# Performance work log

Measured on AMD Instinct MI355X. Metric: run time of the kernel, lower is better.

The kernel has to match this reference:

```python
import jax, jax.numpy as jnp
import numpy as np

B, T, RNN_DIM, ENC_DIM, ATT_DIM, NFILT, KSIZE = 256, 1024, 1024, 512, 128, 32, 31
PAD = (KSIZE - 1) // 2


def setup_inputs() -> dict:
    key = jax.random.key(0)
    ks = jax.random.split(key, 10)
    attn = jax.random.uniform(ks[3], (B, T), dtype=jnp.float32)
    attn = attn / jnp.sum(attn, axis=1, keepdims=True)  # previous-step alignment (sums to 1)
    return {
        "query": jax.random.normal(ks[0], (B, RNN_DIM), dtype=jnp.float32),
        "memory": jax.random.normal(ks[1], (B, T, ENC_DIM), dtype=jnp.float32),
        "processed_memory": jax.random.normal(ks[2], (B, T, ATT_DIM), dtype=jnp.float32),
        "attn_weights": attn,
        "attn_weights_cum": jax.random.uniform(ks[4], (B, T), dtype=jnp.float32),
        "memory_lengths": jax.random.randint(ks[5], (B,), T // 2, T + 1),
        "conv_w": jax.random.normal(ks[6], (NFILT, 2, KSIZE), dtype=jnp.float32) * 0.1,
        "W_loc": jax.random.normal(ks[7], (ATT_DIM, NFILT), dtype=jnp.float32) * 0.1,
        "W_q": jax.random.normal(ks[8], (ATT_DIM, RNN_DIM), dtype=jnp.float32) * 0.03,
        "v_w": jax.random.normal(ks[9], (1, ATT_DIM), dtype=jnp.float32) * 0.1,
        "v_b": jnp.zeros((1,), dtype=jnp.float32),
    }


def reference(query, memory, processed_memory, attn_weights, attn_weights_cum,
              memory_lengths, conv_w, W_loc, W_q, v_w, v_b):
    Tlen = memory.shape[1]
    # [B, 2, T]: stack prev + cumulative alignments
    cat = jnp.stack([attn_weights, attn_weights_cum], axis=1)
    # location conv: Conv1d(2 -> NFILT, k=31, same padding, no bias) -> [B, NFILT, T]
    loc = jax.lax.conv_general_dilated(
        cat, conv_w, window_strides=(1,), padding=[(PAD, PAD)],
        dimension_numbers=("NCH", "OIH", "NCH"))
    # location_dense: [B, T, ATT_DIM]
    processed_location = jnp.einsum("bct,ac->bta", loc, W_loc)
    # query projection: [B, 1, ATT_DIM]
    processed_query = (query @ W_q.T)[:, None, :]
    # additive energies: v . tanh(q + loc + mem) -> [B, T]
    hidden = jnp.tanh(processed_query + processed_location + processed_memory)
    energies = jnp.einsum("bta,a->bt", hidden, v_w[0]) + v_b[0]
    # mask padded positions (pos >= length) with -inf
    mask = jnp.arange(Tlen)[None, :] >= memory_lengths[:, None]
    energies = jnp.where(mask, -jnp.inf, energies)
    new_attn = jax.nn.softmax(energies, axis=1)
    new_cum = attn_weights_cum + new_attn
    # context: [B, ENC_DIM]
    context = jnp.einsum("bt,bte->be", new_attn, memory)
    return context, new_attn, new_cum
```

## Files before the change

### kernel.cpp

```cpp
#include <hip/hip_runtime.h>
#include <math.h>

#define Bc 256
#define Tc 1024
#define RNN_DIMc 1024
#define ENC_DIMc 512
#define ATT_DIMc 128
#define NFILTc 32
#define KSIZEc 31
#define PADc 15

typedef float f4v __attribute__((ext_vector_type(4)));

__device__ __forceinline__ float fast_tanh(float x) {
    x = fminf(15.f, fmaxf(-15.f, x));
    float z = __expf(2.f * x);
    return (z - 1.f) / (z + 1.f);
}

__device__ __forceinline__ float wave_reduce_max(float x) {
#pragma unroll
    for (int off = 32; off > 0; off >>= 1) x = fmaxf(x, __shfl_xor(x, off, 64));
    return x;
}

__device__ __forceinline__ float wave_reduce_sum(float x) {
#pragma unroll
    for (int off = 32; off > 0; off >>= 1) x += __shfl_xor(x, off, 64);
    return x;
}

__global__ __launch_bounds__(128) void qproj_k(const float* __restrict__ query,
                                               const float* __restrict__ W_q,
                                               float* __restrict__ pq) {
    const int b = blockIdx.x;
    __shared__ float q[RNN_DIMc];
    for (int i = threadIdx.x; i < RNN_DIMc; i += 128) q[i] = query[b * RNN_DIMc + i];
    __syncthreads();
    const float* w = W_q + (size_t)threadIdx.x * RNN_DIMc;
    float acc = 0.f;
#pragma unroll 4
    for (int r = 0; r < RNN_DIMc; r += 4) {
        float4 wv = *(const float4*)(w + r);
        acc = fmaf(wv.x, q[r + 0], acc);
        acc = fmaf(wv.y, q[r + 1], acc);
        acc = fmaf(wv.z, q[r + 2], acc);
        acc = fmaf(wv.w, q[r + 3], acc);
    }
    pq[b * ATT_DIMc + threadIdx.x] = acc;
}

__global__ __launch_bounds__(1024) void lsa_fused(
    const float* __restrict__ memory, const float* __restrict__ pm,
    const float* __restrict__ attn_w, const float* __restrict__ cum_w,
    const int* __restrict__ lens, const float* __restrict__ conv_w,
    const float* __restrict__ W_loc, const float* __restrict__ pq_g,
    const float* __restrict__ v_w, const float* __restrict__ v_b,
    float* __restrict__ ctx, float* __restrict__ out_attn, float* __restrict__ out_cum) {
    const int b = blockIdx.x;
    const int tid = threadIdx.x;
    const int len = lens[b];

    __shared__ float s_pq[ATT_DIMc];
    __shared__ float s_win0[Tc + 2 * PADc];
    __shared__ float s_win1[Tc + 2 * PADc];
    __shared__ float s_attn[Tc];
    __shared__ float s_redm[16];
    __shared__ float s_reds[16];
    __shared__ float s_scratch[8][ENC_DIMc];

    if (tid < ATT_DIMc) s_pq[tid] = pq_g[b * ATT_DIMc + tid];
    for (int i = tid; i < Tc + 2 * PADc; i += 1024) {
        int tt = i - PADc;
        bool ok = (tt >= 0) && (tt < Tc);
        s_win0[i] = ok ? attn_w[b * Tc + tt] : 0.f;
        s_win1[i] = ok ? cum_w[b * Tc + tt] : 0.f;
    }
    __syncthreads();

    const int t = tid;
    float e = -INFINITY;
    if (t < len) {
        float loc[NFILTc];
#pragma unroll
        for (int f = 0; f < NFILTc; ++f) loc[f] = 0.f;
        for (int k = 0; k < KSIZEc; ++k) {
            const float wa = s_win0[t + k];
            const float wc = s_win1[t + k];
#pragma unroll
            for (int f = 0; f < NFILTc; ++f) {
                loc[f] = fmaf(conv_w[f * (2 * KSIZEc) + k], wa, loc[f]);
                loc[f] = fmaf(conv_w[f * (2 * KSIZEc) + KSIZEc + k], wc, loc[f]);
            }
        }

        const float* pmrow = pm + ((size_t)(b * Tc + t)) * ATT_DIMc;
        float acc = 0.f;
#pragma unroll 2
        for (int a = 0; a < ATT_DIMc; a += 4) {
            const f4v pmv = __builtin_nontemporal_load((const f4v*)(pmrow + a));
            const float* wl = W_loc + a * NFILTc;
            float pl0 = 0.f, pl1 = 0.f, pl2 = 0.f, pl3 = 0.f;
#pragma unroll
            for (int f = 0; f < NFILTc; ++f) {
                float lf = loc[f];
                pl0 = fmaf(wl[f], lf, pl0);
                pl1 = fmaf(wl[NFILTc + f], lf, pl1);
                pl2 = fmaf(wl[2 * NFILTc + f], lf, pl2);
                pl3 = fmaf(wl[3 * NFILTc + f], lf, pl3);
            }
            acc = fmaf(v_w[a + 0], fast_tanh(s_pq[a + 0] + pl0 + pmv.x), acc);
            acc = fmaf(v_w[a + 1], fast_tanh(s_pq[a + 1] + pl1 + pmv.y), acc);
            acc = fmaf(v_w[a + 2], fast_tanh(s_pq[a + 2] + pl2 + pmv.z), acc);
            acc = fmaf(v_w[a + 3], fast_tanh(s_pq[a + 3] + pl3 + pmv.w), acc);
        }
        e = acc + v_b[0];
    }

    {
        float m = wave_reduce_max(e);
        if ((tid & 63) == 0) s_redm[tid >> 6] = m;
        __syncthreads();
        float bm = s_redm[0];
#pragma unroll
        for (int j = 1; j < 16; ++j) bm = fmaxf(bm, s_redm[j]);

        float p = __expf(e - bm);
        float s = wave_reduce_sum(p);
        if ((tid & 63) == 0) s_reds[tid >> 6] = s;
        __syncthreads();
        float tot = 0.f;
#pragma unroll
        for (int j = 0; j < 16; ++j) tot += s_reds[j];
        float na = p * (1.f / tot);

        out_attn[b * Tc + t] = na;
        out_cum[b * Tc + t] = s_win1[t + PADc] + na;
        s_attn[t] = na;
    }
    __syncthreads();

    {
        const int tr = tid >> 7;
        const int e4 = (tid & 127) * 4;
        const float* mb = memory + (size_t)b * Tc * ENC_DIMc;
        f4v acc = {0.f, 0.f, 0.f, 0.f};
#pragma unroll 4
        for (int tt = tr; tt < len; tt += 8) {
            const float w = s_attn[tt];
            const f4v mv = __builtin_nontemporal_load((const f4v*)(mb + (size_t)tt * ENC_DIMc + e4));
            acc.x = fmaf(w, mv.x, acc.x);
            acc.y = fmaf(w, mv.y, acc.y);
            acc.z = fmaf(w, mv.z, acc.z);
            acc.w = fmaf(w, mv.w, acc.w);
        }
        *(f4v*)&s_scratch[tr][e4] = acc;
    }
    __syncthreads();
    if (tid < ENC_DIMc) {
        float s = 0.f;
#pragma unroll
        for (int j = 0; j < 8; ++j) s += s_scratch[j][tid];
        ctx[b * ENC_DIMc + tid] = s;
    }
}

extern "C" void kernel_launch(void* const* d_in, const int* in_sizes, int n_in,
                              void* d_out, int out_size, void* d_ws, size_t ws_size,
                              hipStream_t stream) {
    const float* query  = (const float*)d_in[0];
    const float* memory = (const float*)d_in[1];
    const float* pm     = (const float*)d_in[2];
    const float* attn_w = (const float*)d_in[3];
    const float* cum_w  = (const float*)d_in[4];
    const int*   lens   = (const int*)d_in[5];
    const float* conv_w = (const float*)d_in[6];
    const float* W_loc  = (const float*)d_in[7];
    const float* W_q    = (const float*)d_in[8];
    const float* v_w    = (const float*)d_in[9];
    const float* v_b    = (const float*)d_in[10];

    float* out      = (float*)d_out;
    float* ctx      = out;
    float* out_attn = out + Bc * ENC_DIMc;
    float* out_cum  = out + Bc * ENC_DIMc + Bc * Tc;

    float* pq = (float*)d_ws;

    qproj_k<<<Bc, 128, 0, stream>>>(query, W_q, pq);
    lsa_fused<<<Bc, 1024, 0, stream>>>(memory, pm, attn_w, cum_w, lens,
                                       conv_w, W_loc, pq, v_w, v_b,
                                       ctx, out_attn, out_cum);
}
```

Before: 816.1 us.

## Fuse query projection into main attention kernel and widen context reduction

Removes the separate qproj kernel and computes the query projection inside each block: 8 threads per attention dim split the 1024-wide dot product and combine partials with wave shuffles. This drops one kernel launch and the global round trip for the projected query. The context stage now uses 16 row groups with 8 contiguous floats per thread instead of 8 row groups with 4, which means more loads in flight but doubles the shared-memory scratch to 32KB and may lower occupancy.

```diff
diff --git a/kernel.cpp b/kernel.cpp
--- a/kernel.cpp
+++ b/kernel.cpp
@@ -30,51 +30,54 @@
     return x;
 }
 
-__global__ __launch_bounds__(128) void qproj_k(const float* __restrict__ query,
-                                               const float* __restrict__ W_q,
-                                               float* __restrict__ pq) {
-    const int b = blockIdx.x;
-    __shared__ float q[RNN_DIMc];
-    for (int i = threadIdx.x; i < RNN_DIMc; i += 128) q[i] = query[b * RNN_DIMc + i];
-    __syncthreads();
-    const float* w = W_q + (size_t)threadIdx.x * RNN_DIMc;
-    float acc = 0.f;
-#pragma unroll 4
-    for (int r = 0; r < RNN_DIMc; r += 4) {
-        float4 wv = *(const float4*)(w + r);
-        acc = fmaf(wv.x, q[r + 0], acc);
-        acc = fmaf(wv.y, q[r + 1], acc);
-        acc = fmaf(wv.z, q[r + 2], acc);
-        acc = fmaf(wv.w, q[r + 3], acc);
-    }
-    pq[b * ATT_DIMc + threadIdx.x] = acc;
-}
-
 __global__ __launch_bounds__(1024) void lsa_fused(
-    const float* __restrict__ memory, const float* __restrict__ pm,
-    const float* __restrict__ attn_w, const float* __restrict__ cum_w,
-    const int* __restrict__ lens, const float* __restrict__ conv_w,
-    const float* __restrict__ W_loc, const float* __restrict__ pq_g,
-    const float* __restrict__ v_w, const float* __restrict__ v_b,
-    float* __restrict__ ctx, float* __restrict__ out_attn, float* __restrict__ out_cum) {
+    const float* __restrict__ query, const float* __restrict__ memory,
+    const float* __restrict__ pm, const float* __restrict__ attn_w,
+    const float* __restrict__ cum_w, const int* __restrict__ lens,
+    const float* __restrict__ conv_w, const float* __restrict__ W_loc,
+    const float* __restrict__ W_q, const float* __restrict__ v_w,
+    const float* __restrict__ v_b, float* __restrict__ ctx,
+    float* __restrict__ out_attn, float* __restrict__ out_cum) {
     const int b = blockIdx.x;
     const int tid = threadIdx.x;
     const int len = lens[b];
 
+    __shared__ float s_q[RNN_DIMc];
     __shared__ float s_pq[ATT_DIMc];
     __shared__ float s_win0[Tc + 2 * PADc];
     __shared__ float s_win1[Tc + 2 * PADc];
     __shared__ float s_attn[Tc];
     __shared__ float s_redm[16];
     __shared__ float s_reds[16];
-    __shared__ float s_scratch[8][ENC_DIMc];
-
-    if (tid < ATT_DIMc) s_pq[tid] = pq_g[b * ATT_DIMc + tid];
+    __shared__ float s_ctx[16][ENC_DIMc];
+
+    s_q[tid] = query[b * RNN_DIMc + tid];
     for (int i = tid; i < Tc + 2 * PADc; i += 1024) {
         int tt = i - PADc;
         bool ok = (tt >= 0) && (tt < Tc);
         s_win0[i] = ok ? attn_w[b * Tc + tt] : 0.f;
         s_win1[i] = ok ? cum_w[b * Tc + tt] : 0.f;
+    }
+    __syncthreads();
+
+    {
+        const int a = tid >> 3;
+        const int c = tid & 7;
+        const float* w = W_q + (size_t)a * RNN_DIMc;
+        float acc = 0.f;
+#pragma unroll 4
+        for (int j = 0; j < 32; ++j) {
+            const int r = c * 4 + j * 32;
+            float4 wv = *(const float4*)(w + r);
+            acc = fmaf(wv.x, s_q[r + 0], acc);
+            acc = fmaf(wv.y, s_q[r + 1], acc);
+            acc = fmaf(wv.z, s_q[r + 2], acc);
+            acc = fmaf(wv.w, s_q[r + 3], acc);
+        }
+        acc += __shfl_xor(acc, 1, 64);
+        acc += __shfl_xor(acc, 2, 64);
+        acc += __shfl_xor(acc, 4, 64);
+        if (c == 0) s_pq[a] = acc;
     }
     __syncthreads();
 
@@ -141,26 +144,34 @@
     __syncthreads();
 
     {
-        const int tr = tid >> 7;
-        const int e4 = (tid & 127) * 4;
+        const int tr = tid >> 6;
+        const int e8 = (tid & 63) * 8;
         const float* mb = memory + (size_t)b * Tc * ENC_DIMc;
-        f4v acc = {0.f, 0.f, 0.f, 0.f};
+        f4v acc0 = {0.f, 0.f, 0.f, 0.f};
+        f4v acc1 = {0.f, 0.f, 0.f, 0.f};
 #pragma unroll 4
-        for (int tt = tr; tt < len; tt += 8) {
+        for (int tt = tr; tt < len; tt += 16) {
             const float w = s_attn[tt];
-            const f4v mv = __builtin_nontemporal_load((const f4v*)(mb + (size_t)tt * ENC_DIMc + e4));
-            acc.x = fmaf(w, mv.x, acc.x);
-            acc.y = fmaf(w, mv.y, acc.y);
-            acc.z = fmaf(w, mv.z, acc.z);
-            acc.w = fmaf(w, mv.w, acc.w);
-        }
-        *(f4v*)&s_scratch[tr][e4] = acc;
+            const float* row = mb + (size_t)tt * ENC_DIMc + e8;
+            const f4v m0 = __builtin_nontemporal_load((const f4v*)(row));
+            const f4v m1 = __builtin_nontemporal_load((const f4v*)(row + 4));
+            acc0.x = fmaf(w, m0.x, acc0.x);
+            acc0.y = fmaf(w, m0.y, acc0.y);
+            acc0.z = fmaf(w, m0.z, acc0.z);
+            acc0.w = fmaf(w, m0.w, acc0.w);
+            acc1.x = fmaf(w, m1.x, acc1.x);
+            acc1.y = fmaf(w, m1.y, acc1.y);
+            acc1.z = fmaf(w, m1.z, acc1.z);
+            acc1.w = fmaf(w, m1.w, acc1.w);
+        }
+        *(f4v*)&s_ctx[tr][e8] = acc0;
+        *(f4v*)&s_ctx[tr][e8 + 4] = acc1;
     }
     __syncthreads();
     if (tid < ENC_DIMc) {
         float s = 0.f;
 #pragma unroll
-        for (int j = 0; j < 8; ++j) s += s_scratch[j][tid];
+        for (int j = 0; j < 16; ++j) s += s_ctx[j][tid];
         ctx[b * ENC_DIMc + tid] = s;
     }
 }
@@ -185,10 +196,8 @@
     float* out_attn = out + Bc * ENC_DIMc;
     float* out_cum  = out + Bc * ENC_DIMc + Bc * Tc;
 
-    float* pq = (float*)d_ws;
-
-    qproj_k<<<Bc, 128, 0, stream>>>(query, W_q, pq);
-    lsa_fused<<<Bc, 1024, 0, stream>>>(memory, pm, attn_w, cum_w, lens,
-                                       conv_w, W_loc, pq, v_w, v_b,
+
+    lsa_fused<<<Bc, 1024, 0, stream>>>(query, memory, pm, attn_w, cum_w, lens,
+                                       conv_w, W_loc, W_q, v_w, v_b,
                                        ctx, out_attn, out_cum);
 }
```

Result: faster. 799.3 us (-2.1%).

## Split each batch row into four time-quarter blocks with split-softmax combine kernel

Applied to the files above, without the earlier changes.

The single 1024-thread block per batch row becomes four 256-thread blocks, one per quarter of the time axis. Each block computes local softmax max and sum, unnormalized probabilities and a partial context, and writes them to workspace. A new combine kernel rescales the partials into the final attention, cumulative weights and context. This gives 1024 smaller blocks instead of 256 large ones, improving occupancy and load balance across CUs, at the cost of an extra launch and extra workspace traffic.

```diff
diff --git a/kernel.cpp b/kernel.cpp
--- a/kernel.cpp
+++ b/kernel.cpp
@@ -9,6 +9,8 @@
 #define NFILTc 32
 #define KSIZEc 31
 #define PADc 15
+#define NQ 4
+#define QT (Tc / NQ)
 
 typedef float f4v __attribute__((ext_vector_type(4)));
 
@@ -50,50 +52,52 @@
     pq[b * ATT_DIMc + threadIdx.x] = acc;
 }
 
-__global__ __launch_bounds__(1024) void lsa_fused(
+__global__ __launch_bounds__(256, 4) void lsa_main(
     const float* __restrict__ memory, const float* __restrict__ pm,
     const float* __restrict__ attn_w, const float* __restrict__ cum_w,
     const int* __restrict__ lens, const float* __restrict__ conv_w,
     const float* __restrict__ W_loc, const float* __restrict__ pq_g,
     const float* __restrict__ v_w, const float* __restrict__ v_b,
-    float* __restrict__ ctx, float* __restrict__ out_attn, float* __restrict__ out_cum) {
-    const int b = blockIdx.x;
+    float* __restrict__ p_buf, float* __restrict__ m_buf,
+    float* __restrict__ s_buf, float* __restrict__ ctx_buf) {
+    const int bq = blockIdx.x;
+    const int b = bq >> 2;
+    const int q = bq & 3;
+    const int t0 = q * QT;
     const int tid = threadIdx.x;
     const int len = lens[b];
 
     __shared__ float s_pq[ATT_DIMc];
-    __shared__ float s_win0[Tc + 2 * PADc];
-    __shared__ float s_win1[Tc + 2 * PADc];
-    __shared__ float s_attn[Tc];
-    __shared__ float s_redm[16];
-    __shared__ float s_reds[16];
-    __shared__ float s_scratch[8][ENC_DIMc];
+    __shared__ float s_win0[QT + 2 * PADc];
+    __shared__ float s_win1[QT + 2 * PADc];
+    __shared__ float s_attn[QT];
+    __shared__ float s_red[4];
+    __shared__ float s_ctx[4][ENC_DIMc];
 
     if (tid < ATT_DIMc) s_pq[tid] = pq_g[b * ATT_DIMc + tid];
-    for (int i = tid; i < Tc + 2 * PADc; i += 1024) {
-        int tt = i - PADc;
+    for (int i = tid; i < QT + 2 * PADc; i += 256) {
+        int tt = t0 + i - PADc;
         bool ok = (tt >= 0) && (tt < Tc);
         s_win0[i] = ok ? attn_w[b * Tc + tt] : 0.f;
         s_win1[i] = ok ? cum_w[b * Tc + tt] : 0.f;
     }
     __syncthreads();
 
-    const int t = tid;
+    const int t = t0 + tid;
     float e = -INFINITY;
     if (t < len) {
         float loc[NFILTc];
 #pragma unroll
         for (int f = 0; f < NFILTc; ++f) loc[f] = 0.f;
         for (int k = 0; k < KSIZEc; ++k) {
-            const float wa = s_win0[t + k];
-            const float wc = s_win1[t + k];
+            const float wa = s_win0[tid + k];
+            const float wc = s_win1[tid + k];
 #pragma unroll
             for (int f = 0; f < NFILTc; ++f) {
                 loc[f] = fmaf(conv_w[f * (2 * KSIZEc) + k], wa, loc[f]);
                 loc[f] = fmaf(conv_w[f * (2 * KSIZEc) + KSIZEc + k], wc, loc[f]);
             }
         }
-
         const float* pmrow = pm + ((size_t)(b * Tc + t)) * ATT_DIMc;
         float acc = 0.f;
 #pragma unroll 2
@@ -119,49 +123,94 @@
 
     {
         float m = wave_reduce_max(e);
-        if ((tid & 63) == 0) s_redm[tid >> 6] = m;
+        if ((tid & 63) == 0) s_red[tid >> 6] = m;
         __syncthreads();
-        float bm = s_redm[0];
-#pragma unroll
-        for (int j = 1; j < 16; ++j) bm = fmaxf(bm, s_redm[j]);
-
-        float p = __expf(e - bm);
+        const float mq = fmaxf(fmaxf(s_red[0], s_red[1]), fmaxf(s_red[2], s_red[3]));
+        const float p = (t < len) ? __expf(e - mq) : 0.f;
         float s = wave_reduce_sum(p);
-        if ((tid & 63) == 0) s_reds[tid >> 6] = s;
         __syncthreads();
-        float tot = 0.f;
-#pragma unroll
-        for (int j = 0; j < 16; ++j) tot += s_reds[j];
-        float na = p * (1.f / tot);
-
-        out_attn[b * Tc + t] = na;
-        out_cum[b * Tc + t] = s_win1[t + PADc] + na;
-        s_attn[t] = na;
+        if ((tid & 63) == 0) s_red[tid >> 6] = s;
+        __syncthreads();
+        const float sq = s_red[0] + s_red[1] + s_red[2] + s_red[3];
+        p_buf[b * Tc + t] = p;
+        s_attn[tid] = p;
+        if (tid == 0) {
+            m_buf[b * NQ + q] = mq;
+            s_buf[b * NQ + q] = sq;
+        }
     }
     __syncthreads();
 
     {
-        const int tr = tid >> 7;
-        const int e4 = (tid & 127) * 4;
-        const float* mb = memory + (size_t)b * Tc * ENC_DIMc;
-        f4v acc = {0.f, 0.f, 0.f, 0.f};
+        const int tr = tid >> 6;
+        const int e8 = (tid & 63) * 8;
+        const float* mb = memory + (size_t)b * Tc * ENC_DIMc + (size_t)t0 * ENC_DIMc;
+        int lim = len - t0;
+        lim = lim < 0 ? 0 : (lim > QT ? QT : lim);
+        f4v acc0 = {0.f, 0.f, 0.f, 0.f};
+        f4v acc1 = {0.f, 0.f, 0.f, 0.f};
 #pragma unroll 4
-        for (int tt = tr; tt < len; tt += 8) {
+        for (int tt = tr; tt < lim; tt += 4) {
             const float w = s_attn[tt];
-            const f4v mv = __builtin_nontemporal_load((const f4v*)(mb + (size_t)tt * ENC_DIMc + e4));
-            acc.x = fmaf(w, mv.x, acc.x);
-            acc.y = fmaf(w, mv.y, acc.y);
-            acc.z = fmaf(w, mv.z, acc.z);
-            acc.w = fmaf(w, mv.w, acc.w);
-        }
-        *(f4v*)&s_scratch[tr][e4] = acc;
-    }
-    __syncthreads();
+            const float* row = mb + (size_t)tt * ENC_DIMc + e8;
+            const f4v m0 = __builtin_nontemporal_load((const f4v*)(row));
+            const f4v m1 = __builtin_nontemporal_load((const f4v*)(row + 4));
+            acc0.x = fmaf(w, m0.x, acc0.x);
+            acc0.y = fmaf(w, m0.y, acc0.y);
+            acc0.z = fmaf(w, m0.z, acc0.z);
+            acc0.w = fmaf(w, m0.w, acc0.w);
+            acc1.x = fmaf(w, m1.x, acc1.x);
+            acc1.y = fmaf(w, m1.y, acc1.y);
+            acc1.z = fmaf(w, m1.z, acc1.z);
+            acc1.w = fmaf(w, m1.w, acc1.w);
+        }
+        *(f4v*)&s_ctx[tr][e8] = acc0;
+        *(f4v*)&s_ctx[tr][e8 + 4] = acc1;
+    }
+    __syncthreads();
+    for (int e2 = tid; e2 < ENC_DIMc; e2 += 256) {
+        float v = s_ctx[0][e2] + s_ctx[1][e2] + s_ctx[2][e2] + s_ctx[3][e2];
+        ctx_buf[(size_t)(b * NQ + q) * ENC_DIMc + e2] = v;
+    }
+}
+
+__global__ __launch_bounds__(512) void lsa_comb(
+    const float* __restrict__ p_buf, const float* __restrict__ m_buf,
+    const float* __restrict__ s_buf, const float* __restrict__ ctx_buf,
+    const float* __restrict__ cum_w, float* __restrict__ ctx,
+    float* __restrict__ out_attn, float* __restrict__ out_cum) {
+    const int b = blockIdx.x;
+    const int tid = threadIdx.x;
+
+    const float m0 = m_buf[b * NQ + 0], m1 = m_buf[b * NQ + 1];
+    const float m2 = m_buf[b * NQ + 2], m3 = m_buf[b * NQ + 3];
+    const float M = fmaxf(fmaxf(m0, m1), fmaxf(m2, m3));
+    const float ex0 = (m0 == -INFINITY) ? 0.f : __expf(m0 - M);
+    const float ex1 = (m1 == -INFINITY) ? 0.f : __expf(m1 - M);
+    const float ex2 = (m2 == -INFINITY) ? 0.f : __expf(m2 - M);
+    const float ex3 = (m3 == -INFINITY) ? 0.f : __expf(m3 - M);
+    const float S = s_buf[b * NQ + 0] * ex0 + s_buf[b * NQ + 1] * ex1 +
+                    s_buf[b * NQ + 2] * ex2 + s_buf[b * NQ + 3] * ex3;
+    const float inv = 1.f / S;
+
+    {
+        const int tA = tid;
+        const float exA = (tA >> 8) ? ex1 : ex0;
+        const float naA = p_buf[b * Tc + tA] * exA * inv;
+        out_attn[b * Tc + tA] = naA;
+        out_cum[b * Tc + tA] = cum_w[b * Tc + tA] + naA;
+
+        const int tB = tid + 512;
+        const float exB = (tid >> 8) ? ex3 : ex2;
+        const float naB = p_buf[b * Tc + tB] * exB * inv;
+        out_attn[b * Tc + tB] = naB;
+        out_cum[b * Tc + tB] = cum_w[b * Tc + tB] + naB;
+    }
     if (tid < ENC_DIMc) {
-        float s = 0.f;
-#pragma unroll
-        for (int j = 0; j < 8; ++j) s += s_scratch[j][tid];
-        ctx[b * ENC_DIMc + tid] = s;
+        const size_t base = (size_t)(b * NQ) * ENC_DIMc + tid;
+        float v = ctx_buf[base] * ex0 + ctx_buf[base + ENC_DIMc] * ex1 +
+                  ctx_buf[base + 2 * ENC_DIMc] * ex2 + ctx_buf[base + 3 * ENC_DIMc] * ex3;
+        ctx[b * ENC_DIMc + tid] = v * inv;
     }
 }
 
@@ -185,10 +234,17 @@
     float* out_attn = out + Bc * ENC_DIMc;
     float* out_cum  = out + Bc * ENC_DIMc + Bc * Tc;
 
-    float* pq = (float*)d_ws;
+    float* ws      = (float*)d_ws;
+    float* pq      = ws;
+    float* p_buf   = pq + Bc * ATT_DIMc;
+    float* m_buf   = p_buf + Bc * Tc;
+    float* s_buf   = m_buf + Bc * NQ;
+    float* ctx_buf = s_buf + Bc * NQ;
 
     qproj_k<<<Bc, 128, 0, stream>>>(query, W_q, pq);
-    lsa_fused<<<Bc, 1024, 0, stream>>>(memory, pm, attn_w, cum_w, lens,
-                                       conv_w, W_loc, pq, v_w, v_b,
-                                       ctx, out_attn, out_cum);
-}
+    lsa_main<<<Bc * NQ, 256, 0, stream>>>(memory, pm, attn_w, cum_w, lens,
+                                          conv_w, W_loc, pq, v_w, v_b,
+                                          p_buf, m_buf, s_buf, ctx_buf);
+    lsa_comb<<<Bc, 512, 0, stream>>>(p_buf, m_buf, s_buf, ctx_buf, cum_w,
+                                     ctx, out_attn, out_cum);
+}
```

New measurement: 839.0 us. 1.03x slower.
